# Kernel optimization log

Measured on AMD Instinct MI355X. Metric: run time of the kernel, lower is better.

## Reference

```python
import jax, jax.numpy as jnp
import numpy as np

EPS = 1e-5


def _conv1x1(h, w, b):
    # 1x1 conv == per-pixel matmul: (b,c,h,w) x (o,c) -> (b,o,h,w)
    return jnp.einsum('bchw,oc->bohw', h, w) + b[None, :, None, None]


def setup_inputs() -> dict:
    key = jax.random.key(0)
    ks = jax.random.split(key, 7)
    B, C, H, W = 4, 512, 64, 64
    s = 0.02
    return {
        'x': jax.random.normal(ks[0], (B, C, H, W), dtype=jnp.float32),
        'wq': jax.random.normal(ks[1], (C, C), dtype=jnp.float32) * s,
        'bq': jax.random.normal(ks[2], (C,), dtype=jnp.float32) * s,
        'wk': jax.random.normal(ks[3], (C, C), dtype=jnp.float32) * s,
        'bk': jax.random.normal(ks[4], (C,), dtype=jnp.float32) * s,
        'wv': jax.random.normal(ks[5], (C, C), dtype=jnp.float32) * s,
        'bv': jax.random.normal(ks[6], (C,), dtype=jnp.float32) * s,
    }


def reference(x, wq, bq, wk, bk, wv, bv):
    B, C, H, W = x.shape
    # InstanceNorm2d (affine=False): normalize over spatial dims per (b, c)
    mu = jnp.mean(x, axis=(2, 3), keepdims=True)
    var = jnp.var(x, axis=(2, 3), keepdims=True)  # biased, matches torch
    h_ = (x - mu) * jax.lax.rsqrt(var + EPS)

    q = _conv1x1(h_, wq, bq).reshape(B, C, H * W)  # (b, c, n)
    k = _conv1x1(h_, wk, bk).reshape(B, C, H * W)
    v = _conv1x1(h_, wv, bv).reshape(B, C, H * W)

    scale = float(int(C)) ** (-0.5)
    attn = jnp.einsum('bcq,bck->bqk', q, k) * scale  # (b, n_q, n_k)
    attn = jax.nn.softmax(attn, axis=-1)
    # torch: bmm(v, attn.permute(0,2,1)) -> A[b,c,q] = sum_k v[b,c,k] * attn[b,q,k]
    A = jnp.einsum('bck,bqk->bcq', v, attn).reshape(B, C, H, W)
    return x + A
```

## Files before the change

### kernel.cpp

```cpp
#include <hip/hip_runtime.h>
#include <hip/hip_bf16.h>
#include <cstdint>

#define B_ 4
#define C_ 512
#define N_ 4096

typedef unsigned short u16;
typedef unsigned char u8;
typedef __bf16 bf16x8 __attribute__((ext_vector_type(8)));
typedef float f32x4 __attribute__((ext_vector_type(4)));

union U16B { uint4 u; bf16x8 v; };

__device__ __forceinline__ bf16x8 ld16g(const u16* p) {
  U16B t; t.u = *(const uint4*)p; return t.v;
}

__device__ __forceinline__ u16 f2bf(float f) {
  uint32_t u = __builtin_bit_cast(uint32_t, f);
  u = (u + 0x7FFFu + ((u >> 16) & 1u)) >> 16;
  return (u16)u;
}
__device__ __forceinline__ float bf2f(u16 h) {
  uint32_t u = ((uint32_t)h) << 16;
  return __builtin_bit_cast(float, u);
}

__device__ __forceinline__ u8 f2fp8(float f) {
  uint32_t u = __builtin_bit_cast(uint32_t, f);
  uint32_t s = (u >> 24) & 0x80u;
  uint32_t a = u & 0x7FFFFFFFu;
  if (a >= 0x43700000u) return (u8)(s | 0x7E);
  if (a < 0x3C800000u) {
    float af = __builtin_bit_cast(float, a);
    int m = (int)(af * 512.0f + 0.5f);
    return (u8)(s | (uint32_t)m);
  }
  uint32_t r = (a + 0x7FFFFu + ((a >> 20) & 1u)) >> 20;
  return (u8)(s | (r - (120u << 3)));
}

__device__ __forceinline__ u8 f2bf8pos(float f) {
  _Float16 h = (_Float16)f;
  u16 hb = __builtin_bit_cast(unsigned short, h);
  hb = (u16)(hb + 0x7Fu + ((hb >> 8) & 1u));
  return (u8)(hb >> 8);
}

typedef const __attribute__((address_space(1))) uint32_t* gas_p;
typedef __attribute__((address_space(3))) uint32_t* las_p;
__device__ __forceinline__ void gld16(const void* g, void* l) {
  __builtin_amdgcn_global_load_lds((gas_p)g, (las_p)l, 16, 0, 0);
}

#define SCEXP 0.06376149809794171f

__global__ __launch_bounds__(256) void cvt_w(const float* __restrict__ w, u16* __restrict__ o) {
  int i = blockIdx.x * 256 + threadIdx.x;
  float4 v = ((const float4*)w)[i];
  ushort4 r;
  r.x = f2bf(v.x); r.y = f2bf(v.y); r.z = f2bf(v.z); r.w = f2bf(v.w);
  ((ushort4*)o)[i] = r;
}

__global__ __launch_bounds__(1024) void pack_bias(const float* __restrict__ bq,
    const float* __restrict__ bk, float* __restrict__ o) {
  int i = threadIdx.x;
  o[i] = (i < 512) ? bq[i] : bk[i - 512];
}

__global__ __launch_bounds__(256) void inorm_stats(const float* __restrict__ x,
    float* __restrict__ mu, float* __restrict__ rstd) {
  int bc = blockIdx.x;
  const float4* p = (const float4*)(x + (size_t)bc * N_);
  float s = 0.f, ss = 0.f;
  for (int i = threadIdx.x; i < N_ / 4; i += 256) {
    float4 v = p[i];
    s  += v.x + v.y + v.z + v.w;
    ss += v.x * v.x + v.y * v.y + v.z * v.z + v.w * v.w;
  }
#pragma unroll
  for (int off = 32; off > 0; off >>= 1) {
    s  += __shfl_down(s, off);
    ss += __shfl_down(ss, off);
  }
  __shared__ float as_[4], ass_[4];
  if ((threadIdx.x & 63) == 0) { as_[threadIdx.x >> 6] = s; ass_[threadIdx.x >> 6] = ss; }
  __syncthreads();
  if (threadIdx.x == 0) {
    float S  = as_[0] + as_[1] + as_[2] + as_[3];
    float SS = ass_[0] + ass_[1] + ass_[2] + ass_[3];
    float m  = S * (1.f / N_);
    float var = SS * (1.f / N_) - m * m;
    mu[bc] = m;
    rstd[bc] = rsqrtf(var + 1e-5f);
  }
}

__global__ __launch_bounds__(256) void norm_transpose(const float* __restrict__ x,
    const float* __restrict__ mu, const float* __restrict__ rstd, u16* __restrict__ hT) {
  __shared__ u16 tile[64][66];
  int b = blockIdx.z, c0 = blockIdx.y * 64, n0 = blockIdx.x * 64;
  int tn = threadIdx.x & 63, t4 = threadIdx.x >> 6;
  const float* xb = x + ((size_t)b * C_ + c0) * N_ + n0;
#pragma unroll
  for (int it = 0; it < 16; ++it) {
    int c = t4 + it * 4;
    float m  = mu[b * C_ + c0 + c];
    float rs = rstd[b * C_ + c0 + c];
    tile[c][tn] = f2bf((xb[(size_t)c * N_ + tn] - m) * rs);
  }
  __syncthreads();
  u16* hTb = hT + ((size_t)b * N_ + n0) * C_ + c0;
#pragma unroll
  for (int it = 0; it < 16; ++it) {
    int n = t4 + it * 4;
    hTb[(size_t)n * C_ + tn] = tile[tn][n];
  }
}

#define EPI_QK8  2
#define EPI_V8   3

template<int EPI>
__global__ __launch_bounds__(256) void gemm128(
    const u16* __restrict__ A, const u16* __restrict__ B,
    const float* __restrict__ aux, void* __restrict__ Out,
    int klen, int lda, int ldb, int ldo,
    long sAz, long sBz, long sOz)
{
  int z = blockIdx.z;
  const u16* Ab = A + (size_t)z * sAz;
  const u16* Bb = B + (size_t)z * sBz;
  int m0 = blockIdx.x * 128, n0 = blockIdx.y * 128;
  int t = threadIdx.x, w = t >> 6, l = t & 63;
  int wr = w >> 1, wc = w & 1;
  int l16 = l & 15, lg = l >> 4;

  __shared__ char smem[65536];

  int srow = t >> 3;
  int scol = ((t & 7) << 4) ^ ((srow & 7) << 4);
  size_t ldaB = (size_t)lda * 2, ldbB = (size_t)ldb * 2;

  f32x4 acc[4][4] = {};
  int nsteps = klen >> 6;

#define STAGE(step, d) {                                                     \
    size_t kbyte = (size_t)(step) * 128 + scol;                              \
    char* lb = smem + (d) * 32768;                                           \
    _Pragma("unroll")                                                        \
    for (int i = 0; i < 4; ++i) {                                            \
      int row = i * 32 + srow;                                               \
      gld16((const char*)Ab + (size_t)(m0 + row) * ldaB + kbyte,             \
            lb + (size_t)(i * 256 + t) * 16);                                \
      gld16((const char*)Bb + (size_t)(n0 + row) * ldbB + kbyte,             \
            lb + 16384 + (size_t)(i * 256 + t) * 16);                        \
    }                                                                        \
  }

  STAGE(0, 0);
  __syncthreads();
  int cur = 0;
  int sw = (l16 & 7) << 4;
  for (int s = 0; s < nsteps; ++s) {
    if (s + 1 < nsteps) STAGE(s + 1, cur ^ 1);
    const char* Al = smem + cur * 32768;
    const char* Bl = Al + 16384;
#pragma unroll
    for (int kc = 0; kc < 2; ++kc) {
      int cb = (kc * 64 + lg * 16) ^ sw;
      bf16x8 af[4], bf[4];
#pragma unroll
      for (int mf = 0; mf < 4; ++mf)
        af[mf] = *(const bf16x8*)(Al + (wr * 64 + mf * 16 + l16) * 128 + cb);
#pragma unroll
      for (int nf = 0; nf < 4; ++nf)
        bf[nf] = *(const bf16x8*)(Bl + (wc * 64 + nf * 16 + l16) * 128 + cb);
#pragma unroll
      for (int mf = 0; mf < 4; ++mf)
#pragma unroll
        for (int nf = 0; nf < 4; ++nf)
          acc[mf][nf] = __builtin_amdgcn_mfma_f32_16x16x32_bf16(af[mf], bf[nf], acc[mf][nf], 0, 0, 0);
    }
    __syncthreads();
    cur ^= 1;
  }
#undef STAGE

  u8* ob = (u8*)Out + (size_t)z * sOz;
  char* sb = smem;
  if constexpr (EPI == EPI_QK8) {
    float bc[4];
#pragma unroll
    for (int nf = 0; nf < 4; ++nf) bc[nf] = aux[n0 + wc * 64 + nf * 16 + l16];
#pragma unroll
    for (int mf = 0; mf < 4; ++mf) {
#pragma unroll
      for (int r = 0; r < 4; ++r) {
        int rowl = wr * 64 + mf * 16 + lg * 4 + r;
#pragma unroll
        for (int nf = 0; nf < 4; ++nf) {
          int cl = wc * 64 + nf * 16 + l16;
          int w6 = cl & 63;
          int clp = (cl & 64) | (((w6 >> 3) & 3) * 16) | (((w6 >> 5) & 1) * 8) | (w6 & 7);
          sb[rowl * 128 + clp] = (char)f2fp8(acc[mf][nf][r] + bc[nf]);
        }
      }
    }
    __syncthreads();
#pragma unroll
    for (int it = 0; it < 4; ++it) {
      int idx = it * 256 + t;
      int row = idx >> 3, seg = idx & 7;
      *(uint4*)(ob + (size_t)(m0 + row) * ldo + n0 + seg * 16) =
          *(const uint4*)(sb + row * 128 + seg * 16);
    }
  } else {
#pragma unroll
    for (int mf = 0; mf < 4; ++mf) {
#pragma unroll
      for (int r = 0; r < 4; ++r) {
        int rowl = wr * 64 + mf * 16 + lg * 4 + r;
        float brow = aux[m0 + rowl];
        uint32_t pk = 0;
#pragma unroll
        for (int nf = 0; nf < 4; ++nf)
          pk |= (uint32_t)f2fp8(acc[mf][nf][r] + brow) << (8 * nf);
        int blk = (wc ^ ((rowl >> 2) & 1)) << 6;
        *(uint32_t*)(sb + rowl * 128 + blk + l16 * 4) = pk;
      }
    }
    __syncthreads();
#pragma unroll
    for (int it = 0; it < 4; ++it) {
      int idx = it * 256 + t;
      int row = idx >> 3, seg = idx & 7;
      int blk = ((seg >> 2) ^ ((row >> 2) & 1)) << 6;
      *(uint4*)(ob + (size_t)(m0 + row) * ldo + n0 + seg * 16) =
          *(const uint4*)(sb + row * 128 + blk + (seg & 3) * 16);
    }
  }
}

__global__ __launch_bounds__(512, 3) void exp8(
    const u8* __restrict__ qk8, float* __restrict__ dsumAll, u8* __restrict__ Pall)
{
  int fid = blockIdx.x;
  int rid = (fid & 7) * 256 + (fid >> 3);
  int z = rid >> 9;
  int r9 = rid & 511;
  int c2 = r9 >> 8;
  int r8 = r9 & 255;
  int sm = r8 >> 6, w6s = r8 & 63;
  int m0 = (c2 * 16 + (sm >> 1) * 8 + (w6s >> 3)) * 128;
  int n0 = ((sm & 1) * 8 + (w6s & 7)) * 256;

  const u8* Ab = qk8 + (size_t)z * ((size_t)N_ * 1024);
  const u8* Bb = Ab + 512;
  float* dsum = dsumAll + (size_t)z * N_;
  u8* Pp = Pall + (size_t)z * (size_t)N_ * N_;

  int t = threadIdx.x, w = t >> 6, l = t & 63;
  int wr = w >> 2, wc = w & 3;
  int l16 = l & 15, lg = l >> 4;

  __shared__ char smem[49152];

  f32x4 acc[4][4] = {};
  int rg = ((lg ^ ((l16 >> 1) & 3)) & 3) << 4;

#define STG8(step, lb) {                                                     \
    size_t kb = (size_t)(step) * 64;                                         \
    {                                                                        \
      int row = t >> 2, g = t & 3;                                           \
      int sg = (g ^ ((row >> 1) & 3)) << 4;                                  \
      gld16((const char*)Ab + (size_t)(m0 + row) * 1024 + kb + sg,           \
            (lb) + (size_t)t * 16);                                          \
    }                                                                        \
    _Pragma("unroll")                                                        \
    for (int i = 0; i < 2; ++i) {                                            \
      int s2 = i * 512 + t;                                                  \
      int row = s2 >> 2, g = s2 & 3;                                         \
      int sg = (g ^ ((row >> 1) & 3)) << 4;                                  \
      gld16((const char*)Bb + (size_t)(n0 + row) * 1024 + kb + sg,           \
            (lb) + 8192 + (size_t)s2 * 16);                                  \
    }                                                                        \
  }

#define COMP8(lb) {                                                          \
    const char* Al = (lb);                                                   \
    const char* Bl = (lb) + 8192;                                            \
    uint4 af[4], bf[4];                                                      \
    _Pragma("unroll")                                                        \
    for (int mf = 0; mf < 4; ++mf)                                           \
      af[mf] = *(const uint4*)(Al + (wr * 64 + mf * 16 + l16) * 64 + rg);    \
    _Pragma("unroll")                                                        \
    for (int nf = 0; nf < 4; ++nf)                                           \
      bf[nf] = *(const uint4*)(Bl + (wc * 64 + nf * 16 + l16) * 64 + rg);    \
    _Pragma("unroll")                                                        \
    for (int kk = 0; kk < 2; ++kk) {                                         \
      _Pragma("unroll")                                                      \
      for (int mf = 0; mf < 4; ++mf) {                                       \
        long long a8 = ((long long)(kk ? af[mf].w : af[mf].y) << 32) |       \
                       (unsigned int)(kk ? af[mf].z : af[mf].x);             \
        _Pragma("unroll")                                                    \
        for (int nf = 0; nf < 4; ++nf) {                                     \
          long long b8 = ((long long)(kk ? bf[nf].w : bf[nf].y) << 32) |     \
                         (unsigned int)(kk ? bf[nf].z : bf[nf].x);           \
          acc[mf][nf] = __builtin_amdgcn_mfma_f32_16x16x32_fp8_fp8(          \
              a8, b8, acc[mf][nf], 0, 0, 0);                                 \
        }                                                                    \
      }                                                                      \
    }                                                                        \
  }

  char* buf0 = smem;
  char* buf1 = smem + 24576;

  STG8(0, buf0);
#pragma unroll
  for (int s = 0; s < 8; ++s) {
    char* cb = (s & 1) ? buf1 : buf0;
    char* nb = (s & 1) ? buf0 : buf1;
    if (s < 7) {
      STG8(s + 1, nb);
      asm volatile("s_waitcnt vmcnt(3)" ::: "memory");
    } else {
      asm volatile("s_waitcnt vmcnt(0)" ::: "memory");
    }
    __builtin_amdgcn_s_barrier();
    __builtin_amdgcn_sched_barrier(0);
    COMP8(cb);
    __builtin_amdgcn_sched_barrier(0);
    __builtin_amdgcn_s_barrier();
  }
#undef STG8
#undef COMP8

#pragma unroll
  for (int mf = 0; mf < 4; ++mf) {
#pragma unroll
    for (int r = 0; r < 4; ++r) {
      int row = wr * 64 + mf * 16 + lg * 4 + r;
      float rs = 0.f;
      uint32_t pk = 0;
#pragma unroll
      for (int nf = 0; nf < 4; ++nf) {
        float p = __builtin_amdgcn_exp2f(acc[mf][nf][r] * SCEXP);
        rs += p;
        pk |= (uint32_t)f2bf8pos(p) << (8 * nf);
      }
      int blk = (wc ^ lg) << 6;
      *(uint32_t*)(smem + row * 256 + blk + l16 * 4) = pk;
      rs += __shfl_xor(rs, 1); rs += __shfl_xor(rs, 2);
      rs += __shfl_xor(rs, 4); rs += __shfl_xor(rs, 8);
      if (l16 == 0) atomicAdd(&dsum[m0 + row], rs);
    }
  }
  __syncthreads();
#pragma unroll
  for (int it = 0; it < 4; ++it) {
    int idx = it * 512 + t;
    int row = idx >> 4, seg = idx & 15;
    int blk = ((seg >> 2) ^ ((row >> 2) & 3)) << 6;
    *(uint4*)(Pp + ((size_t)(m0 + row) * N_ + n0 + seg * 16)) =
        *(const uint4*)(smem + row * 256 + blk + (seg & 3) * 16);
  }
}

__global__ __launch_bounds__(256, 4) void pv8(
    const u8* __restrict__ vM8, const u8* __restrict__ P8,
    const float* __restrict__ denom, const float* __restrict__ x,
    float* __restrict__ out)
{
  int fid = blockIdx.x;
  int rid = (fid & 7) * 64 + (fid >> 3);
  int z = rid >> 7;
  int r7 = rid & 127;
  int n0 = (r7 >> 2) * 128;
  int m0 = (r7 & 3) * 128;

  const u8* Ab = vM8 + (size_t)z * ((size_t)C_ * N_);
  const u8* Bb = P8 + (size_t)z * ((size_t)N_ * N_);
  const float* db = denom + (size_t)z * N_;
  const float* xb = x + (size_t)z * ((size_t)C_ * N_);
  float* ob = out + (size_t)z * ((size_t)C_ * N_);

  int t = threadIdx.x, w = t >> 6, l = t & 63;
  int wr = w >> 1, wc = w & 1;
  int l16 = l & 15, lg = l >> 4;

  __shared__ char smem[32768];

  f32x4 acc[4][4] = {};
  int rg = ((lg ^ ((l16 >> 1) & 3)) & 3) << 4;

#define STGP(step, lb) {                                                     \
    size_t kb = (size_t)(step) * 64;                                         \
    _Pragma("unroll")                                                        \
    for (int i = 0; i < 2; ++i) {                                            \
      int s2 = i * 256 + t;                                                  \
      int row = s2 >> 2, g = s2 & 3;                                         \
      int sg = (g ^ ((row >> 1) & 3)) << 4;                                  \
      gld16((const char*)Ab + (size_t)(m0 + row) * N_ + kb + sg,             \
            (lb) + (size_t)s2 * 16);                                         \
      gld16((const char*)Bb + (size_t)(n0 + row) * N_ + kb + sg,             \
            (lb) + 8192 + (size_t)s2 * 16);                                  \
    }                                                                        \
  }

#define COMPP(lb) {                                                          \
    const char* Al = (lb);                                                   \
    const char* Bl = (lb) + 8192;                                            \
    uint4 af[4], bf[4];                                                      \
    _Pragma("unroll")                                                        \
    for (int mf = 0; mf < 4; ++mf)                                           \
      af[mf] = *(const uint4*)(Al + (wr * 64 + mf * 16 + l16) * 64 + rg);    \
    _Pragma("unroll")                                                        \
    for (int nf = 0; nf < 4; ++nf)                                           \
      bf[nf] = *(const uint4*)(Bl + (wc * 64 + nf * 16 + l16) * 64 + rg);    \
    _Pragma("unroll")                                                        \
    for (int kk = 0; kk < 2; ++kk) {                                         \
      _Pragma("unroll")                                                      \
      for (int mf = 0; mf < 4; ++mf) {                                       \
        long long a8 = ((long long)(kk ? af[mf].w : af[mf].y) << 32) |       \
                       (unsigned int)(kk ? af[mf].z : af[mf].x);             \
        _Pragma("unroll")                                                    \
        for (int nf = 0; nf < 4; ++nf) {                                     \
          long long b8 = ((long long)(kk ? bf[nf].w : bf[nf].y) << 32) |     \
                         (unsigned int)(kk ? bf[nf].z : bf[nf].x);           \
          acc[mf][nf] = __builtin_amdgcn_mfma_f32_16x16x32_fp8_bf8(          \
              a8, b8, acc[mf][nf], 0, 0, 0);                                 \
        }                                                                    \
      }                                                                      \
    }                                                                        \
  }

  char* buf0 = smem;
  char* buf1 = smem + 16384;

  STGP(0, buf0);
#pragma unroll 2
  for (int s = 0; s < 64; ++s) {
    char* cb = (s & 1) ? buf1 : buf0;
    char* nb = (s & 1) ? buf0 : buf1;
    if (s < 63) {
      STGP(s + 1, nb);
      asm volatile("s_waitcnt vmcnt(4)" ::: "memory");
    } else {
      asm volatile("s_waitcnt vmcnt(0)" ::: "memory");
    }
    __builtin_amdgcn_s_barrier();
    __builtin_amdgcn_sched_barrier(0);
    COMPP(cb);
    __builtin_amdgcn_sched_barrier(0);
    __builtin_amdgcn_s_barrier();
  }
#undef STGP
#undef COMPP

  float rd[4];
#pragma unroll
  for (int nf = 0; nf < 4; ++nf)
    rd[nf] = 1.0f / db[n0 + wc * 64 + nf * 16 + l16];
#pragma unroll
  for (int mf = 0; mf < 4; ++mf) {
#pragma unroll
    for (int r = 0; r < 4; ++r) {
      int row = m0 + wr * 64 + mf * 16 + lg * 4 + r;
#pragma unroll
      for (int nf = 0; nf < 4; ++nf) {
        int col = n0 + wc * 64 + nf * 16 + l16;
        size_t o = (size_t)row * N_ + col;
        ob[o] = xb[o] + acc[mf][nf][r] * rd[nf];
      }
    }
  }
}

__global__ __launch_bounds__(256) void gemm_abT(
    const u16* __restrict__ A, const u16* __restrict__ Bm,
    const float* __restrict__ bias, u16* __restrict__ out,
    int ldo, int bias_is_row)
{
  int w = threadIdx.x >> 6, l = threadIdx.x & 63;
  int l16 = l & 15, lg = l >> 4;
  int m0 = blockIdx.x * 128 + (w >> 1) * 64;
  int n0 = blockIdx.y * 128 + (w & 1) * 64;
  f32x4 acc[4][4] = {};
  const u16* Ab = A  + (size_t)(m0 + l16) * 512 + lg * 8;
  const u16* Bb = Bm + (size_t)(n0 + l16) * 512 + lg * 8;
  for (int kc = 0; kc < 512; kc += 32) {
    bf16x8 af[4], bf[4];
#pragma unroll
    for (int i = 0; i < 4; ++i) af[i] = ld16g(Ab + (size_t)(i * 16) * 512 + kc);
#pragma unroll
    for (int j = 0; j < 4; ++j) bf[j] = ld16g(Bb + (size_t)(j * 16) * 512 + kc);
#pragma unroll
    for (int i = 0; i < 4; ++i)
#pragma unroll
      for (int j = 0; j < 4; ++j)
        acc[i][j] = __builtin_amdgcn_mfma_f32_16x16x32_bf16(af[i], bf[j], acc[i][j], 0, 0, 0);
  }
#pragma unroll
  for (int i = 0; i < 4; ++i) {
#pragma unroll
    for (int j = 0; j < 4; ++j) {
      int col = n0 + j * 16 + l16;
#pragma unroll
      for (int r = 0; r < 4; ++r) {
        int row = m0 + i * 16 + lg * 4 + r;
        float v = acc[i][j][r] + (bias_is_row ? bias[row] : bias[col]);
        out[(size_t)row * ldo + col] = f2bf(v);
      }
    }
  }
}

#define NQ 32
#define NKB 64
__global__ __launch_bounds__(512) void attn_kernel(
    const u16* __restrict__ qT, const u16* __restrict__ kT, const u16* __restrict__ vM,
    const float* __restrict__ x, float* __restrict__ out)
{
  int b = blockIdx.y;
  int nq0 = blockIdx.x * NQ;
  const u16* qTb = qT + (size_t)b * N_ * C_;
  const u16* kTb = kT + (size_t)b * N_ * C_;
  const u16* vb  = vM + (size_t)b * C_ * N_;
  const float* xb = x + (size_t)b * C_ * N_;
  float* ob = out + (size_t)b * C_ * N_;

  int tid = threadIdx.x;
  int w = tid >> 6, l = tid & 63, l16 = l & 15, lg = l >> 4;
  int nqf = w & 1, nkf = w >> 1;
  int c0 = w * 64;

  __shared__ u16 qlds[32][520];
  __shared__ u16 Plds[32][72];
  __shared__ float dpart[32][16];
  __shared__ float dfin[32];

  for (int idx = tid; idx < 32 * 64; idx += 512) {
    int row = idx >> 6, cg = idx & 63;
    *(uint4*)&qlds[row][cg * 8] = *(const uint4*)(qTb + (size_t)(nq0 + row) * C_ + cg * 8);
  }
  __syncthreads();

  f32x4 acc[2][4] = {};
  float dreg = 0.f;
  int drow = tid >> 4, dcol = (tid & 15) * 4;

  for (int nk0 = 0; nk0 < N_; nk0 += NKB) {
    f32x4 s = {0.f, 0.f, 0.f, 0.f};
    const u16* krow = kTb + (size_t)(nk0 + nkf * 16 + l16) * C_ + lg * 8;
#pragma unroll 4
    for (int kc = 0; kc < 16; ++kc) {
      U16B tq; tq.u = *(const uint4*)&qlds[nqf * 16 + l16][kc * 32 + lg * 8];
      bf16x8 kf = ld16g(krow + kc * 32);
      s = __builtin_amdgcn_mfma_f32_16x16x32_bf16(tq.v, kf, s, 0, 0, 0);
    }
    __syncthreads();
#pragma unroll
    for (int r = 0; r < 4; ++r) {
      float p = __builtin_amdgcn_exp2f(s[r] * SCEXP);
      Plds[nqf * 16 + lg * 4 + r][nkf * 16 + l16] = f2bf(p);
    }
    __syncthreads();
#pragma unroll
    for (int r = 0; r < 4; ++r) dreg += bf2f(Plds[drow][dcol + r]);
#pragma unroll
    for (int kk = 0; kk < 2; ++kk) {
      bf16x8 pf[2];
#pragma unroll
      for (int i = 0; i < 2; ++i) {
        U16B t2; t2.u = *(const uint4*)&Plds[i * 16 + l16][kk * 32 + lg * 8];
        pf[i] = t2.v;
      }
#pragma unroll
      for (int j = 0; j < 4; ++j) {
        bf16x8 vf = ld16g(vb + (size_t)(c0 + j * 16 + l16) * N_ + nk0 + kk * 32 + lg * 8);
#pragma unroll
        for (int i = 0; i < 2; ++i)
          acc[i][j] = __builtin_amdgcn_mfma_f32_16x16x32_bf16(pf[i], vf, acc[i][j], 0, 0, 0);
      }
    }
  }

  dpart[drow][tid & 15] = dreg;
  __syncthreads();
  if (tid < 32) {
    float s2 = 0.f;
#pragma unroll
    for (int g = 0; g < 16; ++g) s2 += dpart[tid][g];
    dfin[tid] = s2;
  }
  __syncthreads();

#pragma unroll
  for (int i = 0; i < 2; ++i) {
    float dinv[4];
#pragma unroll
    for (int r = 0; r < 4; ++r) dinv[r] = 1.f / dfin[i * 16 + lg * 4 + r];
    int nbase = nq0 + i * 16 + lg * 4;
#pragma unroll
    for (int j = 0; j < 4; ++j) {
      int c = c0 + j * 16 + l16;
      float4 xv = *(const float4*)(xb + (size_t)c * N_ + nbase);
      float4 o;
      o.x = xv.x + acc[i][j][0] * dinv[0];
      o.y = xv.y + acc[i][j][1] * dinv[1];
      o.z = xv.z + acc[i][j][2] * dinv[2];
      o.w = xv.w + acc[i][j][3] * dinv[3];
      *(float4*)(ob + (size_t)c * N_ + nbase) = o;
    }
  }
}

extern "C" void kernel_launch(void* const* d_in, const int* in_sizes, int n_in,
                              void* d_out, int out_size, void* d_ws, size_t ws_size,
                              hipStream_t stream) {
  (void)in_sizes; (void)n_in; (void)out_size;
  const float* x  = (const float*)d_in[0];
  const float* wq = (const float*)d_in[1];
  const float* bq = (const float*)d_in[2];
  const float* wk = (const float*)d_in[3];
  const float* bk = (const float*)d_in[4];
  const float* wv = (const float*)d_in[5];
  const float* bv = (const float*)d_in[6];
  float* out = (float*)d_out;
  char* ws = (char*)d_ws;

  const size_t NC = (size_t)N_ * C_;
  const size_t NEED = 136380416;

  if (ws_size >= NEED) {
    u16*   wbf_q = (u16*)(ws);
    u16*   wbf_k = (u16*)(ws + 524288);
    u16*   wbf_v = (u16*)(ws + 1048576);
    float* bqk   = (float*)(ws + 1572864);
    float* mu    = (float*)(ws + 1581056);
    float* rstd  = (float*)(ws + 1589248);
    u16*   hT    = (u16*)(ws + 1597440);
    u8*    qk8   = (u8*)(ws + 18874368);
    u8*    vM8   = (u8*)(ws + 52428800);
    float* denom = (float*)(ws + 69206016);
    u8*    P8    = (u8*)(ws + 69271552);

    cvt_w<<<256, 256, 0, stream>>>(wq, wbf_q);
    cvt_w<<<256, 256, 0, stream>>>(wk, wbf_k);
    cvt_w<<<256, 256, 0, stream>>>(wv, wbf_v);
    pack_bias<<<1, 1024, 0, stream>>>(bq, bk, bqk);
    inorm_stats<<<B_ * C_, 256, 0, stream>>>(x, mu, rstd);
    norm_transpose<<<dim3(N_ / 64, C_ / 64, B_), 256, 0, stream>>>(x, mu, rstd, hT);
    hipMemsetAsync(denom, 0, 4 * N_ * sizeof(float), stream);

    gemm128<EPI_QK8><<<dim3(32, 8, 4), 256, 0, stream>>>(
        hT, wbf_q, bqk, qk8, 512, 512, 512, 1024, (long)NC, 0, (long)N_ * 1024);
    gemm128<EPI_V8><<<dim3(4, 32, 4), 256, 0, stream>>>(
        wbf_v, hT, bv, vM8, 512, 512, 512, 4096, 0, (long)NC, (long)NC);

    exp8<<<2048, 512, 0, stream>>>(qk8, denom, P8);

    pv8<<<512, 256, 0, stream>>>(vM8, P8, denom, x, out);
  } else {
    u16*   wbf_q = (u16*)(ws);
    u16*   wbf_k = (u16*)(ws + 524288);
    u16*   wbf_v = (u16*)(ws + 1048576);
    float* mu    = (float*)(ws + 1572864);
    float* rstd  = (float*)(ws + 1581056);
    u16*   hT    = (u16*)(ws + 1589248);
    u16*   qT    = (u16*)(ws + 18366464);
    u16*   kT    = (u16*)(ws + 35143680);
    u16*   vM    = (u16*)(ws + 51920896);

    cvt_w<<<256, 256, 0, stream>>>(wq, wbf_q);
    cvt_w<<<256, 256, 0, stream>>>(wk, wbf_k);
    cvt_w<<<256, 256, 0, stream>>>(wv, wbf_v);
    inorm_stats<<<B_ * C_, 256, 0, stream>>>(x, mu, rstd);
    norm_transpose<<<dim3(N_ / 64, C_ / 64, B_), 256, 0, stream>>>(x, mu, rstd, hT);

    for (int b = 0; b < B_; ++b) {
      const u16* hTb = hT + (size_t)b * NC;
      u16* qTb = qT + (size_t)b * NC;
      u16* kTb = kT + (size_t)b * NC;
      u16* vMb = vM + (size_t)b * NC;
      gemm_abT<<<dim3(N_ / 128, C_ / 128), 256, 0, stream>>>(hTb, wbf_q, bq, qTb, C_, 0);
      gemm_abT<<<dim3(N_ / 128, C_ / 128), 256, 0, stream>>>(hTb, wbf_k, bk, kTb, C_, 0);
      gemm_abT<<<dim3(C_ / 128, N_ / 128), 256, 0, stream>>>(wbf_v, hTb, bv, vMb, N_, 1);
    }
    attn_kernel<<<dim3(N_ / NQ, B_), 512, 0, stream>>>(qT, kT, vM, x, out);
  }
}
```

Before: 222.5 us.

## Switch Q/K/V projections from bf16 to fp8 MFMA with new proj8 kernel

Weights and normalized activations are now converted to fp8, and the Q/K and V projection GEMMs use a new 512-thread fp8 MFMA kernel with 128x256 tiles, replacing the bf16 gemm128. An extra cvt_h8 kernel converts the bf16 transposed activations to fp8. The aim is to halve operand bandwidth and double MFMA throughput in the projections. The cost is one more launch and pass over hT, plus lower precision in Q, K and V.

```diff
diff --git a/kernel.cpp b/kernel.cpp
--- a/kernel.cpp
+++ b/kernel.cpp
@@ -62,6 +62,14 @@
   ushort4 r;
   r.x = f2bf(v.x); r.y = f2bf(v.y); r.z = f2bf(v.z); r.w = f2bf(v.w);
   ((ushort4*)o)[i] = r;
+}
+
+__global__ __launch_bounds__(256) void cvt_w8(const float* __restrict__ w, u8* __restrict__ o) {
+  int i = blockIdx.x * 256 + threadIdx.x;
+  float4 v = ((const float4*)w)[i];
+  uchar4 r;
+  r.x = f2fp8(v.x); r.y = f2fp8(v.y); r.z = f2fp8(v.z); r.w = f2fp8(v.w);
+  ((uchar4*)o)[i] = r;
 }
 
 __global__ __launch_bounds__(1024) void pack_bias(const float* __restrict__ bq,
@@ -120,147 +128,35 @@
   }
 }
 
-#define EPI_QK8  2
-#define EPI_V8   3
+__global__ __launch_bounds__(256) void cvt_h8(const u16* __restrict__ hT, u8* __restrict__ h8) {
+  int i = blockIdx.x * 256 + threadIdx.x;
+  uint4 v = ((const uint4*)hT)[i];
+  uint32_t lo =  (uint32_t)f2fp8(bf2f((u16)(v.x & 0xffff)))
+              | ((uint32_t)f2fp8(bf2f((u16)(v.x >> 16))) << 8)
+              | ((uint32_t)f2fp8(bf2f((u16)(v.y & 0xffff))) << 16)
+              | ((uint32_t)f2fp8(bf2f((u16)(v.y >> 16))) << 24);
+  uint32_t hi =  (uint32_t)f2fp8(bf2f((u16)(v.z & 0xffff)))
+              | ((uint32_t)f2fp8(bf2f((u16)(v.z >> 16))) << 8)
+              | ((uint32_t)f2fp8(bf2f((u16)(v.w & 0xffff))) << 16)
+              | ((uint32_t)f2fp8(bf2f((u16)(v.w >> 16))) << 24);
+  uint2 o; o.x = lo; o.y = hi;
+  ((uint2*)h8)[i] = o;
+}
+
+#define EPI_Q 0
+#define EPI_V 1
 
 template<int EPI>
-__global__ __launch_bounds__(256) void gemm128(
-    const u16* __restrict__ A, const u16* __restrict__ B,
-    const float* __restrict__ aux, void* __restrict__ Out,
-    int klen, int lda, int ldb, int ldo,
-    long sAz, long sBz, long sOz)
+__global__ __launch_bounds__(512, 3) void proj8(
+    const u8* __restrict__ A, const u8* __restrict__ B,
+    const float* __restrict__ aux, u8* __restrict__ Out,
+    long sAz, long sBz, long sOz, int ldo)
 {
   int z = blockIdx.z;
-  const u16* Ab = A + (size_t)z * sAz;
-  const u16* Bb = B + (size_t)z * sBz;
-  int m0 = blockIdx.x * 128, n0 = blockIdx.y * 128;
-  int t = threadIdx.x, w = t >> 6, l = t & 63;
-  int wr = w >> 1, wc = w & 1;
-  int l16 = l & 15, lg = l >> 4;
-
-  __shared__ char smem[65536];
-
-  int srow = t >> 3;
-  int scol = ((t & 7) << 4) ^ ((srow & 7) << 4);
-  size_t ldaB = (size_t)lda * 2, ldbB = (size_t)ldb * 2;
-
-  f32x4 acc[4][4] = {};
-  int nsteps = klen >> 6;
-
-#define STAGE(step, d) {                                                     \
-    size_t kbyte = (size_t)(step) * 128 + scol;                              \
-    char* lb = smem + (d) * 32768;                                           \
-    _Pragma("unroll")                                                        \
-    for (int i = 0; i < 4; ++i) {                                            \
-      int row = i * 32 + srow;                                               \
-      gld16((const char*)Ab + (size_t)(m0 + row) * ldaB + kbyte,             \
-            lb + (size_t)(i * 256 + t) * 16);                                \
-      gld16((const char*)Bb + (size_t)(n0 + row) * ldbB + kbyte,             \
-            lb + 16384 + (size_t)(i * 256 + t) * 16);                        \
-    }                                                                        \
-  }
-
-  STAGE(0, 0);
-  __syncthreads();
-  int cur = 0;
-  int sw = (l16 & 7) << 4;
-  for (int s = 0; s < nsteps; ++s) {
-    if (s + 1 < nsteps) STAGE(s + 1, cur ^ 1);
-    const char* Al = smem + cur * 32768;
-    const char* Bl = Al + 16384;
-#pragma unroll
-    for (int kc = 0; kc < 2; ++kc) {
-      int cb = (kc * 64 + lg * 16) ^ sw;
-      bf16x8 af[4], bf[4];
-#pragma unroll
-      for (int mf = 0; mf < 4; ++mf)
-        af[mf] = *(const bf16x8*)(Al + (wr * 64 + mf * 16 + l16) * 128 + cb);
-#pragma unroll
-      for (int nf = 0; nf < 4; ++nf)
-        bf[nf] = *(const bf16x8*)(Bl + (wc * 64 + nf * 16 + l16) * 128 + cb);
-#pragma unroll
-      for (int mf = 0; mf < 4; ++mf)
-#pragma unroll
-        for (int nf = 0; nf < 4; ++nf)
-          acc[mf][nf] = __builtin_amdgcn_mfma_f32_16x16x32_bf16(af[mf], bf[nf], acc[mf][nf], 0, 0, 0);
-    }
-    __syncthreads();
-    cur ^= 1;
-  }
-#undef STAGE
-
-  u8* ob = (u8*)Out + (size_t)z * sOz;
-  char* sb = smem;
-  if constexpr (EPI == EPI_QK8) {
-    float bc[4];
-#pragma unroll
-    for (int nf = 0; nf < 4; ++nf) bc[nf] = aux[n0 + wc * 64 + nf * 16 + l16];
-#pragma unroll
-    for (int mf = 0; mf < 4; ++mf) {
-#pragma unroll
-      for (int r = 0; r < 4; ++r) {
-        int rowl = wr * 64 + mf * 16 + lg * 4 + r;
-#pragma unroll
-        for (int nf = 0; nf < 4; ++nf) {
-          int cl = wc * 64 + nf * 16 + l16;
-          int w6 = cl & 63;
-          int clp = (cl & 64) | (((w6 >> 3) & 3) * 16) | (((w6 >> 5) & 1) * 8) | (w6 & 7);
-          sb[rowl * 128 + clp] = (char)f2fp8(acc[mf][nf][r] + bc[nf]);
-        }
-      }
-    }
-    __syncthreads();
-#pragma unroll
-    for (int it = 0; it < 4; ++it) {
-      int idx = it * 256 + t;
-      int row = idx >> 3, seg = idx & 7;
-      *(uint4*)(ob + (size_t)(m0 + row) * ldo + n0 + seg * 16) =
-          *(const uint4*)(sb + row * 128 + seg * 16);
-    }
-  } else {
-#pragma unroll
-    for (int mf = 0; mf < 4; ++mf) {
-#pragma unroll
-      for (int r = 0; r < 4; ++r) {
-        int rowl = wr * 64 + mf * 16 + lg * 4 + r;
-        float brow = aux[m0 + rowl];
-        uint32_t pk = 0;
-#pragma unroll
-        for (int nf = 0; nf < 4; ++nf)
-          pk |= (uint32_t)f2fp8(acc[mf][nf][r] + brow) << (8 * nf);
-        int blk = (wc ^ ((rowl >> 2) & 1)) << 6;
-        *(uint32_t*)(sb + rowl * 128 + blk + l16 * 4) = pk;
-      }
-    }
-    __syncthreads();
-#pragma unroll
-    for (int it = 0; it < 4; ++it) {
-      int idx = it * 256 + t;
-      int row = idx >> 3, seg = idx & 7;
-      int blk = ((seg >> 2) ^ ((row >> 2) & 1)) << 6;
-      *(uint4*)(ob + (size_t)(m0 + row) * ldo + n0 + seg * 16) =
-          *(const uint4*)(sb + row * 128 + blk + (seg & 3) * 16);
-    }
-  }
-}
-
-__global__ __launch_bounds__(512, 3) void exp8(
-    const u8* __restrict__ qk8, float* __restrict__ dsumAll, u8* __restrict__ Pall)
-{
-  int fid = blockIdx.x;
-  int rid = (fid & 7) * 256 + (fid >> 3);
-  int z = rid >> 9;
-  int r9 = rid & 511;
-  int c2 = r9 >> 8;
-  int r8 = r9 & 255;
-  int sm = r8 >> 6, w6s = r8 & 63;
-  int m0 = (c2 * 16 + (sm >> 1) * 8 + (w6s >> 3)) * 128;
-  int n0 = ((sm & 1) * 8 + (w6s & 7)) * 256;
-
-  const u8* Ab = qk8 + (size_t)z * ((size_t)N_ * 1024);
-  const u8* Bb = Ab + 512;
-  float* dsum = dsumAll + (size_t)z * N_;
-  u8* Pp = Pall + (size_t)z * (size_t)N_ * N_;
+  const u8* Ab = A + (size_t)z * sAz;
+  const u8* Bb = B + (size_t)z * sBz;
+  u8* ob = Out + (size_t)z * sOz;
+  int m0 = blockIdx.x * 128, n0 = blockIdx.y * 256;
 
   int t = threadIdx.x, w = t >> 6, l = t & 63;
   int wr = w >> 2, wc = w & 3;
@@ -271,12 +167,12 @@
   f32x4 acc[4][4] = {};
   int rg = ((lg ^ ((l16 >> 1) & 3)) & 3) << 4;
 
-#define STG8(step, lb) {                                                     \
+#define STGJ(step, lb) {                                                     \
     size_t kb = (size_t)(step) * 64;                                         \
     {                                                                        \
       int row = t >> 2, g = t & 3;                                           \
       int sg = (g ^ ((row >> 1) & 3)) << 4;                                  \
-      gld16((const char*)Ab + (size_t)(m0 + row) * 1024 + kb + sg,           \
+      gld16((const char*)Ab + (size_t)(m0 + row) * 512 + kb + sg,            \
             (lb) + (size_t)t * 16);                                          \
     }                                                                        \
     _Pragma("unroll")                                                        \
@@ -284,12 +180,12 @@
       int s2 = i * 512 + t;                                                  \
       int row = s2 >> 2, g = s2 & 3;                                         \
       int sg = (g ^ ((row >> 1) & 3)) << 4;                                  \
-      gld16((const char*)Bb + (size_t)(n0 + row) * 1024 + kb + sg,           \
+      gld16((const char*)Bb + (size_t)(n0 + row) * 512 + kb + sg,            \
             (lb) + 8192 + (size_t)s2 * 16);                                  \
     }                                                                        \
   }
 
-#define COMP8(lb) {                                                          \
+#define COMPJ(lb) {                                                          \
     const char* Al = (lb);                                                   \
     const char* Bl = (lb) + 8192;                                            \
     uint4 af[4], bf[4];                                                      \
@@ -319,6 +215,154 @@
   char* buf0 = smem;
   char* buf1 = smem + 24576;
 
+  STGJ(0, buf0);
+#pragma unroll
+  for (int s = 0; s < 8; ++s) {
+    char* cb = (s & 1) ? buf1 : buf0;
+    char* nb = (s & 1) ? buf0 : buf1;
+    if (s < 7) {
+      STGJ(s + 1, nb);
+      asm volatile("s_waitcnt vmcnt(3)" ::: "memory");
+    } else {
+      asm volatile("s_waitcnt vmcnt(0)" ::: "memory");
+    }
+    __builtin_amdgcn_s_barrier();
+    __builtin_amdgcn_sched_barrier(0);
+    COMPJ(cb);
+    __builtin_amdgcn_sched_barrier(0);
+    __builtin_amdgcn_s_barrier();
+  }
+#undef STGJ
+#undef COMPJ
+
+  if constexpr (EPI == EPI_Q) {
+    float bc[4];
+#pragma unroll
+    for (int nf = 0; nf < 4; ++nf) bc[nf] = aux[n0 + wc * 64 + nf * 16 + l16];
+#pragma unroll
+    for (int mf = 0; mf < 4; ++mf) {
+#pragma unroll
+      for (int r = 0; r < 4; ++r) {
+        int row = wr * 64 + mf * 16 + lg * 4 + r;
+        int gx = ((row >> 2) & 3) << 4;
+#pragma unroll
+        for (int nf = 0; nf < 4; ++nf) {
+          int cl = wc * 64 + nf * 16 + l16;
+          smem[row * 256 + (cl ^ gx)] = (char)f2fp8(acc[mf][nf][r] + bc[nf]);
+        }
+      }
+    }
+    __syncthreads();
+#pragma unroll
+    for (int it = 0; it < 4; ++it) {
+      int idx = it * 512 + t;
+      int row = idx >> 4, seg = idx & 15;
+      int gx = ((row >> 2) & 3) << 4;
+      uint4 v = *(const uint4*)(smem + row * 256 + ((seg * 16) ^ gx));
+      *(uint4*)(ob + (size_t)(m0 + row) * ldo + n0 + seg * 16) = v;
+    }
+  } else {
+#pragma unroll
+    for (int mf = 0; mf < 4; ++mf) {
+#pragma unroll
+      for (int r = 0; r < 4; ++r) {
+        int row = wr * 64 + mf * 16 + lg * 4 + r;
+        float brow = aux[m0 + row];
+        uint32_t pk = 0;
+#pragma unroll
+        for (int nf = 0; nf < 4; ++nf)
+          pk |= (uint32_t)f2fp8(acc[mf][nf][r] + brow) << (8 * nf);
+        int blk = (wc ^ lg) << 6;
+        *(uint32_t*)(smem + row * 256 + blk + l16 * 4) = pk;
+      }
+    }
+    __syncthreads();
+#pragma unroll
+    for (int it = 0; it < 4; ++it) {
+      int idx = it * 512 + t;
+      int row = idx >> 4, seg = idx & 15;
+      int blk = ((seg >> 2) ^ ((row >> 2) & 3)) << 6;
+      uint4 v = *(const uint4*)(smem + row * 256 + blk + (seg & 3) * 16);
+      *(uint4*)(ob + (size_t)(m0 + row) * ldo + n0 + seg * 16) = v;
+    }
+  }
+}
+
+__global__ __launch_bounds__(512, 3) void exp8(
+    const u8* __restrict__ qk8, float* __restrict__ dsumAll, u8* __restrict__ Pall)
+{
+  int fid = blockIdx.x;
+  int rid = (fid & 7) * 256 + (fid >> 3);
+  int z = rid >> 9;
+  int r9 = rid & 511;
+  int c2 = r9 >> 8;
+  int r8 = r9 & 255;
+  int sm = r8 >> 6, w6s = r8 & 63;
+  int m0 = (c2 * 16 + (sm >> 1) * 8 + (w6s >> 3)) * 128;
+  int n0 = ((sm & 1) * 8 + (w6s & 7)) * 256;
+
+  const u8* Ab = qk8 + (size_t)z * ((size_t)N_ * 1024);
+  const u8* Bb = Ab + 512;
+  float* dsum = dsumAll + (size_t)z * N_;
+  u8* Pp = Pall + (size_t)z * (size_t)N_ * N_;
+
+  int t = threadIdx.x, w = t >> 6, l = t & 63;
+  int wr = w >> 2, wc = w & 3;
+  int l16 = l & 15, lg = l >> 4;
+
+  __shared__ char smem[49152];
+
+  f32x4 acc[4][4] = {};
+  int rg = ((lg ^ ((l16 >> 1) & 3)) & 3) << 4;
+
+#define STG8(step, lb) {                                                     \
+    size_t kb = (size_t)(step) * 64;                                         \
+    {                                                                        \
+      int row = t >> 2, g = t & 3;                                           \
+      int sg = (g ^ ((row >> 1) & 3)) << 4;                                  \
+      gld16((const char*)Ab + (size_t)(m0 + row) * 1024 + kb + sg,           \
+            (lb) + (size_t)t * 16);                                          \
+    }                                                                        \
+    _Pragma("unroll")                                                        \
+    for (int i = 0; i < 2; ++i) {                                            \
+      int s2 = i * 512 + t;                                                  \
+      int row = s2 >> 2, g = s2 & 3;                                         \
+      int sg = (g ^ ((row >> 1) & 3)) << 4;                                  \
+      gld16((const char*)Bb + (size_t)(n0 + row) * 1024 + kb + sg,           \
+            (lb) + 8192 + (size_t)s2 * 16);                                  \
+    }                                                                        \
+  }
+
+#define COMP8(lb) {                                                          \
+    const char* Al = (lb);                                                   \
+    const char* Bl = (lb) + 8192;                                            \
+    uint4 af[4], bf[4];                                                      \
+    _Pragma("unroll")                                                        \
+    for (int mf = 0; mf < 4; ++mf)                                           \
+      af[mf] = *(const uint4*)(Al + (wr * 64 + mf * 16 + l16) * 64 + rg);    \
+    _Pragma("unroll")                                                        \
+    for (int nf = 0; nf < 4; ++nf)                                           \
+      bf[nf] = *(const uint4*)(Bl + (wc * 64 + nf * 16 + l16) * 64 + rg);    \
+    _Pragma("unroll")                                                        \
+    for (int kk = 0; kk < 2; ++kk) {                                         \
+      _Pragma("unroll")                                                      \
+      for (int mf = 0; mf < 4; ++mf) {                                       \
+        long long a8 = ((long long)(kk ? af[mf].w : af[mf].y) << 32) |       \
+                       (unsigned int)(kk ? af[mf].z : af[mf].x);             \
+        _Pragma("unroll")                                                    \
+        for (int nf = 0; nf < 4; ++nf) {                                     \
+          long long b8 = ((long long)(kk ? bf[nf].w : bf[nf].y) << 32) |     \
+                         (unsigned int)(kk ? bf[nf].z : bf[nf].x);           \
+          acc[mf][nf] = __builtin_amdgcn_mfma_f32_16x16x32_fp8_fp8(          \
+              a8, b8, acc[mf][nf], 0, 0, 0);                                 \
+        }                                                                    \
+      }                                                                      \
+    }                                                                        \
+  }
+
+  char* buf0 = smem;
+  char* buf1 = smem + 24576;
+
   STG8(0, buf0);
 #pragma unroll
   for (int s = 0; s < 8; ++s) {
@@ -634,33 +678,34 @@
   char* ws = (char*)d_ws;
 
   const size_t NC = (size_t)N_ * C_;
-  const size_t NEED = 136380416;
+  const size_t NEED = 118312960;
 
   if (ws_size >= NEED) {
-    u16*   wbf_q = (u16*)(ws);
-    u16*   wbf_k = (u16*)(ws + 524288);
-    u16*   wbf_v = (u16*)(ws + 1048576);
-    float* bqk   = (float*)(ws + 1572864);
-    float* mu    = (float*)(ws + 1581056);
-    float* rstd  = (float*)(ws + 1589248);
-    u16*   hT    = (u16*)(ws + 1597440);
-    u8*    qk8   = (u8*)(ws + 18874368);
-    u8*    vM8   = (u8*)(ws + 52428800);
-    float* denom = (float*)(ws + 69206016);
-    u8*    P8    = (u8*)(ws + 69271552);
-
-    cvt_w<<<256, 256, 0, stream>>>(wq, wbf_q);
-    cvt_w<<<256, 256, 0, stream>>>(wk, wbf_k);
-    cvt_w<<<256, 256, 0, stream>>>(wv, wbf_v);
+    u8*    wqk8  = (u8*)(ws);
+    u8*    wv8   = (u8*)(ws + 524288);
+    float* bqk   = (float*)(ws + 786432);
+    float* mu    = (float*)(ws + 790528);
+    float* rstd  = (float*)(ws + 798720);
+    u16*   hT    = (u16*)(ws + 806912);
+    u8*    h8    = (u8*)(ws + 17584128);
+    u8*    qk8   = (u8*)(ws + 25972736);
+    u8*    vM8   = (u8*)(ws + 42749952);
+    float* denom = (float*)(ws + 51138560);
+    u8*    P8    = (u8*)(ws + 51204096);
+
+    cvt_w8<<<256, 256, 0, stream>>>(wq, wqk8);
+    cvt_w8<<<256, 256, 0, stream>>>(wk, wqk8 + 262144);
+    cvt_w8<<<256, 256, 0, stream>>>(wv, wv8);
     pack_bias<<<1, 1024, 0, stream>>>(bq, bk, bqk);
     inorm_stats<<<B_ * C_, 256, 0, stream>>>(x, mu, rstd);
     norm_transpose<<<dim3(N_ / 64, C_ / 64, B_), 256, 0, stream>>>(x, mu, rstd, hT);
+    cvt_h8<<<4096, 256, 0, stream>>>(hT, h8);
     hipMemsetAsync(denom, 0, 4 * N_ * sizeof(float), stream);
 
-    gemm128<EPI_QK8><<<dim3(32, 8, 4), 256, 0, stream>>>(
-        hT, wbf_q, bqk, qk8, 512, 512, 512, 1024, (long)NC, 0, (long)N_ * 1024);
-    gemm128<EPI_V8><<<dim3(4, 32, 4), 256, 0, stream>>>(
-        wbf_v, hT, bv, vM8, 512, 512, 512, 4096, 0, (long)NC, (long)NC);
+    proj8<EPI_Q><<<dim3(32, 4, 4), 512, 0, stream>>>(
+        h8, wqk8, bqk, qk8, (long)NC, 0, (long)N_ * 1024, 1024);
+    proj8<EPI_V><<<dim3(4, 16, 4), 512, 0, stream>>>(
+        wv8, h8, bv, vM8, 0, (long)NC, (long)NC, 4096);
 
     exp8<<<2048, 512, 0, stream>>>(qk8, denom, P8);
 
```

Result: no change. 221.1 us (-0.6%).
